# Kernel optimization log

Hardware: AMD Instinct MI355X
Metric: run time of the kernel (lower is better)

The kernel has to match this reference:

```python
import jax, jax.numpy as jnp
import numpy as np

B, S, D, H = 2, 2048, 1024, 16  # batch, seq, embed_dim, num_heads
DH = D // H                      # head dim = 64


def setup_inputs() -> dict:
    key = jax.random.key(0)
    kx, kq, kbq, kk, kbk, kv, kbv = jax.random.split(key, 7)
    scale = 1.0 / np.sqrt(D)
    return {
        "x": jax.random.normal(kx, (B, S, D), dtype=jnp.float32),
        "Wq": jax.random.normal(kq, (D, D), dtype=jnp.float32) * scale,
        "bq": jax.random.normal(kbq, (D,), dtype=jnp.float32) * 0.01,
        "Wk": jax.random.normal(kk, (D, D), dtype=jnp.float32) * scale,
        "bk": jax.random.normal(kbk, (D,), dtype=jnp.float32) * 0.01,
        "Wv": jax.random.normal(kv, (D, D), dtype=jnp.float32) * scale,
        "bv": jax.random.normal(kbv, (D,), dtype=jnp.float32) * 0.01,
    }


def reference(x, Wq, bq, Wk, bk, Wv, bv):
    # ooqkv_type == 'q', odeint_method == 'id': q branch = act(Linear(x)), exact GELU (torch nn.GELU default)
    q = jax.nn.gelu(x @ Wq + bq, approximate=False)
    k = x @ Wk + bk
    v = x @ Wv + bv
    # [B, S, D] -> [B, S, H, DH]
    q = q.reshape(B, S, H, DH)
    k = k.reshape(B, S, H, DH)
    v = v.reshape(B, S, H, DH)
    # NOTE: original module has NO 1/sqrt(d) scale — faithful reproduction
    att = jnp.einsum("bqhd,bkhd->bhqk", q, k)
    att = jax.nn.softmax(att, axis=-1)
    out = jnp.einsum("bhqk,bkhd->bqhd", att, v)
    return out.reshape(B, S, D)
```

## Files before the change

kernel.cpp:

```cpp
#include <hip/hip_runtime.h>
#include <math.h>

#define B_  2
#define S_  2048
#define D_  1024
#define H_  16
#define DH_ 64
#define M_  (B_ * S_)

typedef _Float16 half_t;
typedef __attribute__((ext_vector_type(8))) _Float16 h8;
typedef __attribute__((ext_vector_type(4))) _Float16 h4;
typedef __attribute__((ext_vector_type(4))) float   f32x4;

#define LOG2E 1.44269504088896f

__device__ __forceinline__ void gll16(const half_t* g, half_t* l) {
    __builtin_amdgcn_global_load_lds(
        (__attribute__((address_space(1))) const void*)g,
        (__attribute__((address_space(3))) void*)l, 16, 0, 0);
}

__global__ __launch_bounds__(256) void prep_k(
    const float* __restrict__ x, half_t* __restrict__ xh,
    const float* __restrict__ Wq, const float* __restrict__ Wk,
    const float* __restrict__ Wv, half_t* __restrict__ Wt)
{
    const int bx = blockIdx.x;
    if (bx < 2048) {
        const size_t i = ((size_t)bx * 256 + threadIdx.x) * 8;
        const float4 a = *(const float4*)(x + i);
        const float4 b = *(const float4*)(x + i + 4);
        h8 o;
        o[0] = (half_t)a.x; o[1] = (half_t)a.y; o[2] = (half_t)a.z; o[3] = (half_t)a.w;
        o[4] = (half_t)b.x; o[5] = (half_t)b.y; o[6] = (half_t)b.z; o[7] = (half_t)b.w;
        *(h8*)(xh + i) = o;
    } else {
        const int gb    = bx - 2048;
        const int which = gb >> 9;
        const float* __restrict__ W = (which == 0) ? Wq : (which == 1) ? Wk : Wv;
        half_t* __restrict__ T = Wt + (size_t)which * D_ * D_;
        const int gw   = (gb & 511) * 4 + (threadIdx.x >> 6);
        const int lane = threadIdx.x & 63;
        const int n    = (gw & 15) * 64 + lane;
        const int k0   = (gw >> 4) * 8;
        h8 o;
        #pragma unroll
        for (int t = 0; t < 8; ++t) o[t] = (half_t)W[(size_t)(k0 + t) * D_ + n];
        *(h8*)(T + (size_t)n * D_ + k0) = o;
    }
}

__global__ __launch_bounds__(256) void qkv_gemm_f16(
    const half_t* __restrict__ xh, const half_t* __restrict__ Wt,
    const float* __restrict__ bq, const float* __restrict__ bk,
    const float* __restrict__ bv,
    half_t* __restrict__ Qo, half_t* __restrict__ Ko, half_t* __restrict__ Vt)
{
    const int n0g   = blockIdx.x * 128;
    const int which = n0g >> 10;
    const int n0    = n0g & 1023;
    const int m0    = blockIdx.y * 128;
    const half_t* __restrict__ Wp  = Wt + (size_t)which * D_ * D_;
    const float* __restrict__ bias = (which == 0) ? bq : (which == 1) ? bk : bv;

    const int tid = threadIdx.x, lane = tid & 63, wave = tid >> 6;
    const int wm = (wave >> 1) * 64, wn = (wave & 1) * 64;
    const int ln = lane & 15, quad = lane >> 4;

    __shared__ __align__(16) half_t As[128 * 64];
    __shared__ __align__(16) half_t Bs[128 * 64];

    f32x4 acc[4][4];
    #pragma unroll
    for (int i = 0; i < 4; ++i)
        #pragma unroll
        for (int j = 0; j < 4; ++j) acc[i][j] = (f32x4){0.f, 0.f, 0.f, 0.f};

    for (int k0 = 0; k0 < D_; k0 += 64) {
        __syncthreads();
        #pragma unroll
        for (int l = 0; l < 4; ++l) {
            const int c  = tid + l * 256;
            const int r  = c >> 3, c0 = c & 7;
            const int cs = c0 ^ (r & 7);
            gll16(xh + (size_t)(m0 + r) * D_ + k0 + cs * 8, &As[c * 8]);
            gll16(Wp + (size_t)(n0 + r) * D_ + k0 + cs * 8, &Bs[c * 8]);
        }
        __syncthreads();

        #pragma unroll
        for (int kc = 0; kc < 2; ++kc) {
            h8 af[4], bf[4];
            #pragma unroll
            for (int i = 0; i < 4; ++i) {
                const int r = wm + i * 16 + ln;
                af[i] = *(const h8*)&As[r * 64 + (((kc << 2) + quad) ^ (r & 7)) * 8];
            }
            #pragma unroll
            for (int j = 0; j < 4; ++j) {
                const int r = wn + j * 16 + ln;
                bf[j] = *(const h8*)&Bs[r * 64 + (((kc << 2) + quad) ^ (r & 7)) * 8];
            }
            #pragma unroll
            for (int i = 0; i < 4; ++i)
                #pragma unroll
                for (int j = 0; j < 4; ++j)
                    acc[i][j] = __builtin_amdgcn_mfma_f32_16x16x32_f16(
                        af[i], bf[j], acc[i][j], 0, 0, 0);
        }
    }

    if (which == 2) {
        #pragma unroll
        for (int j = 0; j < 4; ++j) {
            const int col = n0 + wn + j * 16 + ln;
            const int h = col >> 6, d = col & 63;
            const float bb = bias[col];
            #pragma unroll
            for (int i = 0; i < 4; ++i) {
                const int sg = m0 + wm + i * 16 + quad * 4;
                const int b  = sg >> 11, srow = sg & 2047;
                h4 pv;
                #pragma unroll
                for (int r = 0; r < 4; ++r) pv[r] = (half_t)(acc[i][j][r] + bb);
                *(h4*)(Vt + (((size_t)(b * H_ + h) * DH_ + d) * S_ + srow)) = pv;
            }
        }
    } else {
        half_t* __restrict__ out = (which == 0) ? Qo : Ko;
        #pragma unroll
        for (int j = 0; j < 4; ++j) {
            const int col = n0 + wn + j * 16 + ln;
            const float bb = bias[col];
            #pragma unroll
            for (int i = 0; i < 4; ++i) {
                #pragma unroll
                for (int r = 0; r < 4; ++r) {
                    const int row = m0 + wm + i * 16 + quad * 4 + r;
                    float t = acc[i][j][r] + bb;
                    if (which == 0) {
                        const float u = t * fmaf(t * t, 0.0356774081f, 0.7978845608f);
                        const float e = __builtin_amdgcn_exp2f(u * -2.88539008178f);
                        t = t * __builtin_amdgcn_rcpf(1.0f + e) * LOG2E;
                    }
                    out[(size_t)row * D_ + col] = (half_t)t;
                }
            }
        }
    }
}

#define ATTN_TILE(KS, VS)                                                     \
    do {                                                                      \
        f32x4 sa[4];                                                          \
        __builtin_amdgcn_s_setprio(1);                                        \
        _Pragma("unroll")                                                     \
        for (int j = 0; j < 4; ++j) {                                         \
            const int rK = j * 16 + ln;                                       \
            const h8 ka0 = *(const h8*)&KS[rK * 64 + ((quad)     ^ (rK & 7)) * 8]; \
            const h8 ka1 = *(const h8*)&KS[rK * 64 + ((quad + 4) ^ (rK & 7)) * 8]; \
            f32x4 t = (f32x4){0.f, 0.f, 0.f, 0.f};                            \
            t = __builtin_amdgcn_mfma_f32_16x16x32_f16(ka0, qa0, t, 0, 0, 0); \
            t = __builtin_amdgcn_mfma_f32_16x16x32_f16(ka1, qa1, t, 0, 0, 0); \
            sa[j] = t;                                                        \
        }                                                                     \
        __builtin_amdgcn_s_setprio(0);                                        \
        float mxa = sa[0][0];                                                 \
        _Pragma("unroll")                                                     \
        for (int j = 0; j < 4; ++j)                                           \
            _Pragma("unroll")                                                 \
            for (int r = 0; r < 4; ++r) mxa = fmaxf(mxa, sa[j][r]);           \
        mxa = fmaxf(mxa, __shfl_xor(mxa, 16, 64));                            \
        mxa = fmaxf(mxa, __shfl_xor(mxa, 32, 64));                            \
        if (__ballot(mxa > m_a)) {                                            \
            const float mna = fmaxf(m_a, mxa);                                \
            const float ala = __builtin_amdgcn_exp2f(m_a - mna);              \
            m_a = mna;                                                        \
            float ra[4];                                                      \
            _Pragma("unroll")                                                 \
            for (int r = 0; r < 4; ++r) ra[r] = __shfl(ala, quad * 4 + r, 64);\
            _Pragma("unroll")                                                 \
            for (int r = 0; r < 4; ++r) {                                     \
                la[r] *= ra[r];                                               \
                _Pragma("unroll")                                             \
                for (int j = 0; j < 4; ++j) Oa[j][r] *= ra[r];                \
            }                                                                 \
        }                                                                     \
        _Pragma("unroll")                                                     \
        for (int j = 0; j < 4; ++j) {                                         \
            h4 pva;                                                           \
            _Pragma("unroll")                                                 \
            for (int r = 0; r < 4; ++r)                                       \
                pva[r] = (half_t)__builtin_amdgcn_exp2f(sa[j][r] - m_a);      \
            *(h4*)&QPs[wave * 16 + ln][j * 16 + quad * 4] = pva;              \
        }                                                                     \
        const h8 pa0 = *(const h8*)&QPs[wave * 16 + ln][quad * 8];            \
        const h8 pa1 = *(const h8*)&QPs[wave * 16 + ln][32 + quad * 8];       \
        __builtin_amdgcn_s_setprio(1);                                        \
        _Pragma("unroll")                                                     \
        for (int j = 0; j < 4; ++j) {                                         \
            const int rV = j * 16 + ln;                                       \
            const h8 vb0 = *(const h8*)&VS[rV * 64 + ((quad)     ^ (rV & 7)) * 8]; \
            const h8 vb1 = *(const h8*)&VS[rV * 64 + ((quad + 4) ^ (rV & 7)) * 8]; \
            Oa[j] = __builtin_amdgcn_mfma_f32_16x16x32_f16(pa0, vb0, Oa[j], 0, 0, 0); \
            Oa[j] = __builtin_amdgcn_mfma_f32_16x16x32_f16(pa1, vb1, Oa[j], 0, 0, 0); \
        }                                                                     \
        la = __builtin_amdgcn_mfma_f32_16x16x32_f16(pa0, ones8, la, 0, 0, 0); \
        la = __builtin_amdgcn_mfma_f32_16x16x32_f16(pa1, ones8, la, 0, 0, 0); \
        __builtin_amdgcn_s_setprio(0);                                        \
    } while (0)

__global__ __launch_bounds__(512) void attn_f16(
    const half_t* __restrict__ Q, const half_t* __restrict__ K,
    const half_t* __restrict__ Vt, float* __restrict__ out)
{
    const int tid  = threadIdx.x;
    const int lane = tid & 63;
    const int wave = tid >> 6;
    const int ln   = lane & 15;
    const int quad = lane >> 4;
    const int bh   = blockIdx.y;
    const int b    = bh >> 4;
    const int h    = bh & 15;
    const int q0   = blockIdx.x * 128;

    const half_t* __restrict__ Qb  = Q  + (size_t)b * S_ * D_ + h * DH_;
    const half_t* __restrict__ Kb  = K  + (size_t)b * S_ * D_ + h * DH_;
    const half_t* __restrict__ Vtb = Vt + (size_t)bh * DH_ * S_;

    __shared__ __align__(16) half_t Ks0[64 * 64];
    __shared__ __align__(16) half_t Vs0[64 * 64];
    __shared__ __align__(16) half_t Ks1[64 * 64];
    __shared__ __align__(16) half_t Vs1[64 * 64];
    __shared__ __align__(16) half_t QPs[128][72];

    const int sr  = tid >> 3, sc0 = tid & 7;
    const int scs = sc0 ^ (sr & 7);
    const half_t* kS = Kb  + (size_t)sr * D_ + scs * 8;
    const half_t* vS = Vtb + (size_t)sr * S_ + scs * 8;
    half_t* const kD0 = &Ks0[tid * 8];
    half_t* const vD0 = &Vs0[tid * 8];
    half_t* const kD1 = &Ks1[tid * 8];
    half_t* const vD1 = &Vs1[tid * 8];

    gll16(kS, kD0); gll16(vS, vD0);
    kS += 64 * D_; vS += 64;

    #pragma unroll
    for (int l = 0; l < 2; ++l) {
        const int c = tid + l * 512;
        const int r = c >> 3, k8 = c & 7;
        *(h8*)&QPs[r][k8 * 8] = *(const h8*)(Qb + (size_t)(q0 + r) * D_ + k8 * 8);
    }
    __syncthreads();
    const h8 qa0 = *(const h8*)&QPs[wave * 16 + ln][quad * 8];
    const h8 qa1 = *(const h8*)&QPs[wave * 16 + ln][32 + quad * 8];

    h8 ones8;
    #pragma unroll
    for (int t = 0; t < 8; ++t) ones8[t] = (half_t)1.0f;

    f32x4 Oa[4];
    #pragma unroll
    for (int j = 0; j < 4; ++j) Oa[j] = (f32x4){0.f, 0.f, 0.f, 0.f};
    f32x4 la = (f32x4){0.f, 0.f, 0.f, 0.f};
    float m_a = -INFINITY;

    for (int it = 0; it < 16; ++it) {
        gll16(kS, kD1); gll16(vS, vD1);
        kS += 64 * D_; vS += 64;
        ATTN_TILE(Ks0, Vs0);
        __syncthreads();

        if (it < 15) {
            gll16(kS, kD0); gll16(vS, vD0);
            kS += 64 * D_; vS += 64;
        }
        ATTN_TILE(Ks1, Vs1);
        __syncthreads();
    }

    #pragma unroll
    for (int r = 0; r < 4; ++r) {
        const float iva = 1.0f / la[r];
        const int rowa = q0 + wave * 16 + quad * 4 + r;
        #pragma unroll
        for (int j = 0; j < 4; ++j)
            out[((size_t)b * S_ + rowa) * D_ + h * DH_ + j * 16 + ln] = Oa[j][r] * iva;
    }
}

extern "C" void kernel_launch(void* const* d_in, const int* in_sizes, int n_in,
                              void* d_out, int out_size, void* d_ws, size_t ws_size,
                              hipStream_t stream) {
    const float* x  = (const float*)d_in[0];
    const float* Wq = (const float*)d_in[1];
    const float* bq = (const float*)d_in[2];
    const float* Wk = (const float*)d_in[3];
    const float* bk = (const float*)d_in[4];
    const float* Wv = (const float*)d_in[5];
    const float* bv = (const float*)d_in[6];
    float* out = (float*)d_out;

    const size_t nmd = (size_t)M_ * D_;
    const size_t ndd = (size_t)D_ * D_;
    half_t* xh  = (half_t*)d_ws;
    half_t* Wt  = xh + nmd;
    half_t* Qh  = Wt + 3 * ndd;
    half_t* Kh  = Qh + nmd;
    half_t* Vtw = Kh + nmd;

    prep_k<<<2048 + 1536, 256, 0, stream>>>(x, xh, Wq, Wk, Wv, Wt);
    qkv_gemm_f16<<<dim3(3 * D_ / 128, M_ / 128), 256, 0, stream>>>(
        xh, Wt, bq, bk, bv, Qh, Kh, Vtw);
    attn_f16<<<dim3(S_ / 128, B_ * H_), 512, 0, stream>>>(Qh, Kh, Vtw, out);
}
```

Baseline: 180.2 us.

## Swizzle block order for XCD locality and stage Q/K epilogue through LDS

Remaps block indices in both the QKV GEMM and attention kernels so that consecutive blocks scheduled on the same XCD (lin&7 grouping) share input tiles, improving L2 reuse on the multi-die MI355X. The GEMM's Q/K epilogue now writes its tile into a padded shared buffer and then emits coalesced 16-byte row stores instead of scattered 2-byte stores. It also hoists the load address computation out of the k-loop. In exchange it adds two barriers and enlarges LDS usage, which may reduce occupancy.

Measured after the change: 178.0 us. About the same (-1.2%).

```diff
diff --git a/kernel.cpp b/kernel.cpp
--- a/kernel.cpp
+++ b/kernel.cpp
@@ -57,10 +57,12 @@
     const float* __restrict__ bv,
     half_t* __restrict__ Qo, half_t* __restrict__ Ko, half_t* __restrict__ Vt)
 {
-    const int n0g   = blockIdx.x * 128;
+    const int lin = blockIdx.y * 24 + blockIdx.x;
+    const int swz = (lin & 7) * 96 + (lin >> 3);
+    const int n0g = (swz % 24) * 128;
+    const int m0  = (swz / 24) * 128;
     const int which = n0g >> 10;
     const int n0    = n0g & 1023;
-    const int m0    = blockIdx.y * 128;
     const half_t* __restrict__ Wp  = Wt + (size_t)which * D_ * D_;
     const float* __restrict__ bias = (which == 0) ? bq : (which == 1) ? bk : bv;
 
@@ -68,8 +70,14 @@
     const int wm = (wave >> 1) * 64, wn = (wave & 1) * 64;
     const int ln = lane & 15, quad = lane >> 4;
 
-    __shared__ __align__(16) half_t As[128 * 64];
-    __shared__ __align__(16) half_t Bs[128 * 64];
+    __shared__ __align__(16) half_t SMEM[128 * 136];
+    half_t* const As = SMEM;
+    half_t* const Bs = SMEM + 128 * 64;
+
+    const int r0  = tid >> 3, c0 = tid & 7;
+    const int cs  = c0 ^ (r0 & 7);
+    const half_t* aS = xh + (size_t)(m0 + r0) * D_ + cs * 8;
+    const half_t* bS = Wp + (size_t)(n0 + r0) * D_ + cs * 8;
 
     f32x4 acc[4][4];
     #pragma unroll
@@ -81,12 +89,10 @@
         __syncthreads();
         #pragma unroll
         for (int l = 0; l < 4; ++l) {
-            const int c  = tid + l * 256;
-            const int r  = c >> 3, c0 = c & 7;
-            const int cs = c0 ^ (r & 7);
-            gll16(xh + (size_t)(m0 + r) * D_ + k0 + cs * 8, &As[c * 8]);
-            gll16(Wp + (size_t)(n0 + r) * D_ + k0 + cs * 8, &Bs[c * 8]);
-        }
+            gll16(aS + (size_t)l * 32 * D_, &As[(tid + l * 256) * 8]);
+            gll16(bS + (size_t)l * 32 * D_, &Bs[(tid + l * 256) * 8]);
+        }
+        aS += 64; bS += 64;
         __syncthreads();
 
         #pragma unroll
@@ -128,25 +134,35 @@
             }
         }
     } else {
-        half_t* __restrict__ out = (which == 0) ? Qo : Ko;
+        half_t* __restrict__ outp = (which == 0) ? Qo : Ko;
+        __syncthreads();
         #pragma unroll
         for (int j = 0; j < 4; ++j) {
-            const int col = n0 + wn + j * 16 + ln;
-            const float bb = bias[col];
+            const int col = wn + j * 16 + ln;
+            const float bb = bias[n0 + col];
             #pragma unroll
             for (int i = 0; i < 4; ++i) {
                 #pragma unroll
                 for (int r = 0; r < 4; ++r) {
-                    const int row = m0 + wm + i * 16 + quad * 4 + r;
+                    const int row = wm + i * 16 + quad * 4 + r;
                     float t = acc[i][j][r] + bb;
                     if (which == 0) {
                         const float u = t * fmaf(t * t, 0.0356774081f, 0.7978845608f);
                         const float e = __builtin_amdgcn_exp2f(u * -2.88539008178f);
                         t = t * __builtin_amdgcn_rcpf(1.0f + e) * LOG2E;
                     }
-                    out[(size_t)row * D_ + col] = (half_t)t;
+                    SMEM[row * 136 + col] = (half_t)t;
                 }
             }
+        }
+        __syncthreads();
+        const int cc = tid & 15;
+        const int rr = tid >> 4;
+        #pragma unroll
+        for (int p = 0; p < 8; ++p) {
+            const int row = p * 16 + rr;
+            const h8 v = *(const h8*)&SMEM[row * 136 + cc * 8];
+            *(h8*)(outp + (size_t)(m0 + row) * D_ + n0 + cc * 8) = v;
         }
     }
 }
@@ -220,10 +236,13 @@
     const int wave = tid >> 6;
     const int ln   = lane & 15;
     const int quad = lane >> 4;
-    const int bh   = blockIdx.y;
-    const int b    = bh >> 4;
-    const int h    = bh & 15;
-    const int q0   = blockIdx.x * 128;
+
+    const int lin = blockIdx.y * 16 + blockIdx.x;
+    const int swz = (lin & 7) * 64 + (lin >> 3);
+    const int bh  = swz >> 4;
+    const int b   = bh >> 4;
+    const int h   = bh & 15;
+    const int q0  = (swz & 15) * 128;
 
     const half_t* __restrict__ Qb  = Q  + (size_t)b * S_ * D_ + h * DH_;
     const half_t* __restrict__ Kb  = K  + (size_t)b * S_ * D_ + h * DH_;
```
